# Performance work log

Hardware: AMD Instinct MI355X
Metric: run time of the kernel (lower is better)

The kernel has to match this reference:

```python
import jax, jax.numpy as jnp
import numpy as np
import math

B, L, D, H = 2, 4096, 1024, 16
DH = D // H


def _build_table(seq_len):
    # Faithful port of build_hierarchical_index_lookup_table (static, host-side).
    assert seq_len & (seq_len - 1) == 0
    levels = int(math.log2(seq_len))
    max_valid = 2 * seq_len - 3
    idx = np.full((seq_len, levels), -1, dtype=np.int64)
    cm = np.zeros((seq_len, levels), dtype=bool)
    for n in range(seq_len):
        c = n
        for lvl in range(levels):
            if lvl == 0:
                nxt = c ^ 1
                pair = c
            else:
                nxt = (c // 2 + seq_len) ^ 1
                pair = c // 2 + seq_len
            if nxt > max_valid:
                break
            if pair < nxt:
                cm[n, lvl] = True
            idx[n, lvl] = nxt
            c = nxt
    return idx, cm


def setup_inputs() -> dict:
    rng = jax.random.key(0)
    ks = jax.random.split(rng, 8)
    s = 0.02  # init scale for weights
    idx, cm = _build_table(L)
    return {
        "query": jax.random.normal(ks[0], (B, L, D), jnp.float32),
        "key": jax.random.normal(ks[1], (B, L, D), jnp.float32),
        "value": jax.random.normal(ks[2], (B, L, D), jnp.float32),
        "Wq": jax.random.normal(ks[3], (D, D), jnp.float32) * s,
        "Wk": jax.random.normal(ks[4], (D, D), jnp.float32) * s,
        "Wv": jax.random.normal(ks[5], (D, D), jnp.float32) * s,
        "Wo": jax.random.normal(ks[6], (D, D), jnp.float32) * s,
        "bo": jax.random.normal(ks[7], (D,), jnp.float32) * s,
        "idx_table": jnp.asarray(idx),        # [L, log2(L)] int64
        "causal_mask": jnp.asarray(cm),       # [L, log2(L)] bool
    }


def reference(query, key, value, Wq, Wk, Wv, Wo, bo, idx_table, causal_mask):
    Bq, Lq, Dm = query.shape
    scale = 1.0 / math.sqrt(DH)

    def heads(x, W):  # nn.Linear (no bias) + split heads -> [B,H,L,Dh]
        return (x @ W.T).reshape(Bq, Lq, H, DH).transpose(0, 2, 1, 3)

    Q = heads(query, Wq)
    K = heads(key, Wk)
    V = heads(value, Wv)

    # Build binary-tree hierarchy. Pair weights come from softmax of ZERO
    # logits (Q_parent starts as zeros in the source), so w0 = w1 = 0.5 exactly.
    Ks, Vs = [K], [V]
    while Ks[-1].shape[2] > 1:
        k, v = Ks[-1], Vs[-1]
        Lc = k.shape[2]
        k2 = k.reshape(Bq, H, Lc // 2, 2, DH)
        v2 = v.reshape(Bq, H, Lc // 2, 2, DH)
        Ks.append(0.5 * (k2[:, :, :, 0] + k2[:, :, :, 1]))
        Vs.append(v2[:, :, :, 0] + v2[:, :, :, 1])
    flatK = jnp.concatenate(Ks, axis=2)  # [B,H,2L-1,Dh]
    flatV = jnp.concatenate(Vs, axis=2)

    # Gather neighbor nodes across levels: [B,H,L,levels,Dh]
    nk = flatK[:, :, idx_table]
    nv = flatV[:, :, idx_table]

    self_logits = jnp.einsum('bhnd,bhnd->bhn', Q, K) * scale
    nbr_logits = jnp.einsum('bhld,bhlnd->bhln', Q, nk) * scale
    nbr_logits = jnp.where(causal_mask[None, None], -jnp.inf, nbr_logits)

    all_logits = jnp.concatenate([self_logits[..., None], nbr_logits], axis=-1)
    w = jax.nn.softmax(all_logits, axis=-1)           # [B,H,L,1+levels]
    all_v = jnp.concatenate([V[:, :, :, None, :], nv], axis=3)
    out = jnp.einsum('bhln,bhlnd->bhld', w, all_v)    # [B,H,L,Dh]
    out = out.transpose(0, 2, 1, 3).reshape(Bq, Lq, Dm)
    return out @ Wo.T + bo
```

## Files before the change

kernel.cpp:

```cpp
#include <hip/hip_runtime.h>
#include <cstdint>
#include <cstddef>


typedef __bf16 bf16;
typedef __bf16 bf16x8 __attribute__((ext_vector_type(8)));
typedef __bf16 bf16x4 __attribute__((ext_vector_type(4)));
typedef float  f32x4  __attribute__((ext_vector_type(4)));

#define L_SEQ  4096
#define NFLAT  8192

__device__ __forceinline__ int off_l(int l) { return 8192 - (8192 >> l); }

__device__ __forceinline__ void glds16(const bf16* g, bf16* l) {
  __builtin_amdgcn_global_load_lds(
      (const __attribute__((address_space(1))) unsigned int*)g,
      (__attribute__((address_space(3))) unsigned int*)l, 16, 0, 0);
}

#define MEMFENCE asm volatile("" ::: "memory")
__device__ __forceinline__ void barrier_raw() {
  MEMFENCE; __builtin_amdgcn_s_barrier(); MEMFENCE;
}

__device__ __forceinline__ int swz(int b) { return b ^ (((b >> 9) & 1) << 5); }
__device__ __forceinline__ int la(int row, int col) {
  return ((((row >> 4) << 1) + (col >> 5)) << 10) + ((row & 15) << 6) + ((col & 31) << 1);
}

__global__ __launch_bounds__(256) void cvt3_kernel(
    const float* __restrict__ a, const float* __restrict__ b, const float* __restrict__ c,
    bf16* __restrict__ x, bf16* __restrict__ y, bf16* __restrict__ z) {
  const int s = blockIdx.y;
  const float* src = (s == 0) ? a : (s == 1) ? b : c;
  bf16*        dst = (s == 0) ? x : (s == 1) ? y : z;
  const int i = blockIdx.x * 256 + threadIdx.x;
  const float4 v = ((const float4*)src)[i];
  bf16x4 o;
  o[0] = (bf16)v.x; o[1] = (bf16)v.y; o[2] = (bf16)v.z; o[3] = (bf16)v.w;
  *(bf16x4*)(dst + (size_t)i * 4) = o;
}

__global__ __launch_bounds__(256) void cvt4_kernel(
    const float* __restrict__ a, const float* __restrict__ b,
    const float* __restrict__ c, const float* __restrict__ d,
    bf16* __restrict__ x, bf16* __restrict__ y, bf16* __restrict__ z, bf16* __restrict__ w) {
  const int s = blockIdx.y;
  const float* src = (s == 0) ? a : (s == 1) ? b : (s == 2) ? c : d;
  bf16*        dst = (s == 0) ? x : (s == 1) ? y : (s == 2) ? z : w;
  const int i = blockIdx.x * 256 + threadIdx.x;
  const float4 v = ((const float4*)src)[i];
  bf16x4 o;
  o[0] = (bf16)v.x; o[1] = (bf16)v.y; o[2] = (bf16)v.z; o[3] = (bf16)v.w;
  *(bf16x4*)(dst + (size_t)i * 4) = o;
}

#define BUFB 49152

__device__ __forceinline__ void stage_tile(const bf16* __restrict__ A,
                                           const bf16* __restrict__ W,
                                           int tm, int tn, int k0,
                                           char* buf, int tid, int wid) {
  bf16* Ad = (bf16*)buf;
  bf16* Bd = (bf16*)(buf + 32768);
#pragma unroll
  for (int i = 0; i < 4; i++) {
    const int d  = i * 8192 + tid * 16;
    const int lb = swz(d);
    const int row = ((lb >> 10) >> 1) * 16 + ((lb >> 6) & 15);
    const int col = ((lb >> 10) & 1) * 32 + ((lb & 63) >> 1);
    glds16(A + (size_t)(tm * 256 + row) * 1024 + k0 + col, Ad + (i * 8192 + wid * 1024) / 2);
  }
#pragma unroll
  for (int i = 0; i < 2; i++) {
    const int d  = i * 8192 + tid * 16;
    const int lb = swz(d);
    const int row = ((lb >> 10) >> 1) * 16 + ((lb >> 6) & 15);
    const int col = ((lb >> 10) & 1) * 32 + ((lb & 63) >> 1);
    glds16(W + (size_t)(tn * 128 + row) * 1024 + k0 + col, Bd + (i * 8192 + wid * 1024) / 2);
  }
}

__device__ __forceinline__ void gemm8_core(const bf16* __restrict__ A,
                                           const bf16* __restrict__ W,
                                           int tm, int tn, char* lds,
                                           f32x4 (&acc)[4][4]) {
  const int tid  = threadIdx.x;
  const int wid  = tid >> 6, lane = tid & 63;
  const int wm   = wid >> 1, wn = wid & 1;
  const int laneR  = lane & 15;
  const int laneC8 = (lane >> 4) * 8;

  char* b0 = lds;
  char* b1 = lds + BUFB;
  char* b2 = lds + 2 * BUFB;

  stage_tile(A, W, tm, tn, 0,  b0, tid, wid);
  stage_tile(A, W, tm, tn, 64, b1, tid, wid);

  for (int u = 0; u < 16; ++u) {
    if (u < 15) asm volatile("s_waitcnt vmcnt(6)" ::: "memory");
    else        asm volatile("s_waitcnt vmcnt(0)" ::: "memory");
    barrier_raw();
    if (u + 2 < 16) stage_tile(A, W, tm, tn, (u + 2) << 6, b2, tid, wid);

    const char* Ab = b0;
    const char* Bb = b0 + 32768;
    bf16x8 af[4][2], bfr[4][2];
#pragma unroll
    for (int f = 0; f < 4; f++)
#pragma unroll
      for (int ks = 0; ks < 2; ks++)
        af[f][ks] = *(const bf16x8*)(Ab + swz(la(wm * 64 + f * 16 + laneR, ks * 32 + laneC8)));
#pragma unroll
    for (int j = 0; j < 4; j++)
#pragma unroll
      for (int ks = 0; ks < 2; ks++)
        bfr[j][ks] = *(const bf16x8*)(Bb + swz(la(wn * 64 + j * 16 + laneR, ks * 32 + laneC8)));

    __builtin_amdgcn_s_setprio(1);
#pragma unroll
    for (int f = 0; f < 4; f++)
#pragma unroll
      for (int j = 0; j < 4; j++)
#pragma unroll
        for (int ks = 0; ks < 2; ks++)
          acc[f][j] = __builtin_amdgcn_mfma_f32_16x16x32_bf16(
              af[f][ks], bfr[j][ks], acc[f][j], 0, 0, 0);
    __builtin_amdgcn_s_setprio(0);

    char* t = b0; b0 = b1; b1 = b2; b2 = t;
  }
}

__global__ __launch_bounds__(512, 2) void gemm8_qkv_kernel(
    const bf16* __restrict__ qx, const bf16* __restrict__ kx, const bf16* __restrict__ vx,
    const bf16* __restrict__ wq, const bf16* __restrict__ wk, const bf16* __restrict__ wv,
    bf16* __restrict__ Qb, bf16* __restrict__ fK, bf16* __restrict__ fV) {
  __shared__ __align__(16) char lds[3 * BUFB];
  const int z = blockIdx.y;
  const bf16* A = (z == 0) ? qx : (z == 1) ? kx : vx;
  const bf16* W = (z == 0) ? wq : (z == 1) ? wk : wv;
  bf16* D       = (z == 0) ? Qb : (z == 1) ? fK : fV;
  const int lstr = (z == 0) ? L_SEQ : NFLAT;
  const int tm = blockIdx.x >> 3, tn = blockIdx.x & 7;
  f32x4 acc[4][4] = {};
  gemm8_core(A, W, tm, tn, lds, acc);
  const int lane = threadIdx.x & 63, wid = threadIdx.x >> 6;
  const int m0 = tm * 256 + (wid >> 1) * 64 + (lane >> 4) * 4;
  const int n0 = tn * 128 + (wid & 1) * 64 + (lane & 15);
#pragma unroll
  for (int i = 0; i < 4; i++)
#pragma unroll
    for (int j = 0; j < 4; j++)
#pragma unroll
      for (int r = 0; r < 4; r++) {
        const int m = m0 + i * 16 + r;
        const int n = n0 + j * 16;
        const int b = m >> 12, l = m & 4095;
        const int h = n >> 6,  dh = n & 63;
        D[((size_t)(b * 16 + h) * lstr + l) * 64 + dh] = (bf16)acc[i][j][r];
      }
}

__global__ __launch_bounds__(512, 2) void gemm8_out_kernel(
    const bf16* __restrict__ Ob, const bf16* __restrict__ wo,
    const float* __restrict__ bo, float* __restrict__ out) {
  __shared__ __align__(16) char lds[3 * BUFB];
  const int tm = blockIdx.x >> 3, tn = blockIdx.x & 7;
  f32x4 acc[4][4] = {};
  gemm8_core(Ob, wo, tm, tn, lds, acc);
  const int lane = threadIdx.x & 63, wid = threadIdx.x >> 6;
  const int m0 = tm * 256 + (wid >> 1) * 64 + (lane >> 4) * 4;
  const int n0 = tn * 128 + (wid & 1) * 64 + (lane & 15);
#pragma unroll
  for (int i = 0; i < 4; i++)
#pragma unroll
    for (int j = 0; j < 4; j++)
#pragma unroll
      for (int r = 0; r < 4; r++) {
        const int m = m0 + i * 16 + r;
        const int n = n0 + j * 16;
        out[(size_t)m * 1024 + n] = acc[i][j][r] + bo[n];
      }
}

__global__ __launch_bounds__(64) void tree_l16(bf16* __restrict__ fK, bf16* __restrict__ fV) {
  __shared__ __align__(16) bf16 Kl[64 * 64];
  __shared__ __align__(16) bf16 Vl[64 * 64];
  const int g = blockIdx.x, bh = blockIdx.y;
  const int lane = threadIdx.x;
  const size_t fb = (size_t)bh * NFLAT * 64;
  const size_t leafbase = fb + (size_t)g * 64 * 64;
#pragma unroll
  for (int it = 0; it < 8; it++) {
    glds16(fK + leafbase + it * 512 + lane * 8, Kl + it * 512);
    glds16(fV + leafbase + it * 512 + lane * 8, Vl + it * 512);
  }
  asm volatile("s_waitcnt vmcnt(0)" ::: "memory");
  __syncthreads();

  float pk[7], pv[7];
#pragma unroll
  for (int i = 0; i < 64; i++) {
    float ck = (float)Kl[i * 64 + lane];
    float cv = (float)Vl[i * 64 + lane];
#pragma unroll
    for (int l = 1; l <= 6; l++) {
      if (((i + 1) & ((1 << l) - 1)) != 0) { pk[l] = ck; pv[l] = cv; break; }
      ck += pk[l]; cv += pv[l];
      const int j = (g * 64 + i) >> l;
      fK[fb + (size_t)(off_l(l) + j) * 64 + lane] = (bf16)(ck * (1.0f / (1 << l)));
      fV[fb + (size_t)(off_l(l) + j) * 64 + lane] = (bf16)cv;
    }
  }
}

__global__ __launch_bounds__(64) void tree_l712(bf16* __restrict__ fK, bf16* __restrict__ fV) {
  __shared__ float Ks[64 * 64];
  __shared__ float Vs[64 * 64];
  const int bh = blockIdx.x, d = threadIdx.x;
  const size_t fb = (size_t)bh * NFLAT * 64;
#pragma unroll 8
  for (int i = 0; i < 64; i++) {
    Ks[i * 64 + d] = (float)fK[fb + (size_t)(8064 + i) * 64 + d];
    Vs[i * 64 + d] = (float)fV[fb + (size_t)(8064 + i) * 64 + d];
  }
#pragma unroll
  for (int l = 7; l <= 12; l++) {
    const int cnt = 4096 >> l;
    for (int j = 0; j < cnt; j++) {
      const float k = (Ks[(2 * j) * 64 + d] + Ks[(2 * j + 1) * 64 + d]) * 0.5f;
      const float v =  Vs[(2 * j) * 64 + d] + Vs[(2 * j + 1) * 64 + d];
      Ks[j * 64 + d] = k;
      Vs[j * 64 + d] = v;
      fK[fb + (size_t)(off_l(l) + j) * 64 + d] = (bf16)k;
      fV[fb + (size_t)(off_l(l) + j) * 64 + d] = (bf16)v;
    }
  }
}

__global__ __launch_bounds__(64) void attn_kernel(
    const bf16* __restrict__ Qb, const bf16* __restrict__ fK,
    const bf16* __restrict__ fV, bf16* __restrict__ Ob) {
  __shared__ __align__(16) unsigned short Kl[132 * 64];
  __shared__ __align__(16) unsigned short Vl[132 * 64];
  const int t0  = blockIdx.x * 64;
  const int bh  = blockIdx.y;
  const int tid = threadIdx.x;
  const size_t fb = (size_t)bh * NFLAT * 64;

  for (int u = tid; u < 132 * 8; u += 64) {
    const int r = u >> 3, c = u & 7;
    int flat;
    if      (r < 64)  flat = t0 + r;
    else if (r < 96)  flat = 4096 + (t0 >> 1) + (r - 64);
    else if (r < 112) flat = 6144 + (t0 >> 2) + (r - 96);
    else if (r < 120) flat = 7168 + (t0 >> 3) + (r - 112);
    else if (r < 124) flat = 7680 + (t0 >> 4) + (r - 120);
    else if (r < 126) flat = 7936 + (t0 >> 5) + (r - 124);
    else { const int l = r - 120; flat = (8192 - (8192 >> l) + (t0 >> l)) ^ 1; }
    const int cc = c ^ (r & 7);
    const uint4 kk = *(const uint4*)((const char*)(fK + fb + (size_t)flat * 64) + c * 16);
    const uint4 vv = *(const uint4*)((const char*)(fV + fb + (size_t)flat * 64) + c * 16);
    *(uint4*)((char*)Kl + r * 128 + cc * 16) = kk;
    *(uint4*)((char*)Vl + r * 128 + cc * 16) = vv;
  }
  __syncthreads();

  const int n = t0 + tid;
  int rows[13];
  rows[0] = tid;
#pragma unroll
  for (int l = 0; l < 12; l++) {
    int r;
    if (l == 0)      r = tid ^ 1;
    else if (l <= 5) r = (128 - (128 >> l)) + (((n >> l) ^ 1) - (t0 >> l));
    else             r = 126 + (l - 6);
    rows[l + 1] = r;
  }

  float q[64];
  const bf16* Qr = Qb + ((size_t)bh * L_SEQ + n) * 64;
#pragma unroll
  for (int c = 0; c < 8; c++) {
    bf16x8 v = *(const bf16x8*)(Qr + c * 8);
#pragma unroll
    for (int j = 0; j < 8; j++) q[c * 8 + j] = (float)v[j];
  }

  float lg[13];
#pragma unroll
  for (int v = 0; v < 13; v++) {
    const int r = rows[v];
    float a = 0.f;
#pragma unroll
    for (int c = 0; c < 8; c++) {
      const int cc = c ^ (r & 7);
      const bf16x8 kv = *(const bf16x8*)((const char*)Kl + r * 128 + cc * 16);
#pragma unroll
      for (int j = 0; j < 8; j++) a += q[c * 8 + j] * (float)kv[j];
    }
    lg[v] = a * 0.125f;
  }
#pragma unroll
  for (int v = 1; v < 13; v++)
    if (!((n >> (v - 1)) & 1)) lg[v] = -1e30f;

  float mx = lg[0];
#pragma unroll
  for (int v = 1; v < 13; v++) mx = fmaxf(mx, lg[v]);
  float w[13], s = 0.f;
#pragma unroll
  for (int v = 0; v < 13; v++) { w[v] = __expf(lg[v] - mx); s += w[v]; }
  const float inv = 1.0f / s;

  float o[64];
#pragma unroll
  for (int d = 0; d < 64; d++) o[d] = 0.f;
#pragma unroll
  for (int v = 0; v < 13; v++) {
    const int r = rows[v];
    const float wv = w[v];
#pragma unroll
    for (int c = 0; c < 8; c++) {
      const int cc = c ^ (r & 7);
      const bf16x8 vv = *(const bf16x8*)((const char*)Vl + r * 128 + cc * 16);
#pragma unroll
      for (int j = 0; j < 8; j++) o[c * 8 + j] += wv * (float)vv[j];
    }
  }

  bf16* Or = Ob + ((size_t)(bh >> 4) * L_SEQ + n) * 1024 + (size_t)(bh & 15) * 64;
#pragma unroll
  for (int c = 0; c < 8; c++) {
    bf16x8 ov;
#pragma unroll
    for (int j = 0; j < 8; j++) ov[j] = (bf16)(o[c * 8 + j] * inv);
    *(bf16x8*)(Or + c * 8) = ov;
  }
}

extern "C" void kernel_launch(void* const* d_in, const int* in_sizes, int n_in,
                              void* d_out, int out_size, void* d_ws, size_t ws_size,
                              hipStream_t stream) {
  const float* query = (const float*)d_in[0];
  const float* key   = (const float*)d_in[1];
  const float* value = (const float*)d_in[2];
  const float* Wq    = (const float*)d_in[3];
  const float* Wk    = (const float*)d_in[4];
  const float* Wv    = (const float*)d_in[5];
  const float* Wo    = (const float*)d_in[6];
  const float* bo    = (const float*)d_in[7];
  float* out = (float*)d_out;

  char* ws = (char*)d_ws;
  size_t off = 0;
  auto take = [&](size_t bytes) -> void* {
    void* p = ws + off;
    off += (bytes + 255) & ~(size_t)255;
    return p;
  };
  const size_t XB = (size_t)8192 * 1024 * 2;
  const size_t WB = (size_t)1024 * 1024 * 2;
  bf16* qx  = (bf16*)take(XB);
  bf16* kx  = (bf16*)take(XB);
  bf16* vx  = (bf16*)take(XB);
  bf16* wqx = (bf16*)take(WB);
  bf16* wkx = (bf16*)take(WB);
  bf16* wvx = (bf16*)take(WB);
  bf16* wox = (bf16*)take(WB);
  bf16* Qb  = (bf16*)take((size_t)32 * L_SEQ * 64 * 2);
  bf16* fK  = (bf16*)take((size_t)32 * NFLAT * 64 * 2);
  bf16* fV  = (bf16*)take((size_t)32 * NFLAT * 64 * 2);
  bf16* Ob  = qx;
  (void)in_sizes; (void)n_in; (void)out_size; (void)ws_size;

  cvt3_kernel<<<dim3(8192, 3), 256, 0, stream>>>(query, key, value, qx, kx, vx);
  cvt4_kernel<<<dim3(1024, 4), 256, 0, stream>>>(Wq, Wk, Wv, Wo, wqx, wkx, wvx, wox);

  gemm8_qkv_kernel<<<dim3(256, 3), 512, 0, stream>>>(qx, kx, vx, wqx, wkx, wvx, Qb, fK, fV);

  tree_l16 <<<dim3(64, 32), 64, 0, stream>>>(fK, fV);
  tree_l712<<<32, 64, 0, stream>>>(fK, fV);

  attn_kernel<<<dim3(64, 32), 64, 0, stream>>>(Qb, fK, fV, Ob);

  gemm8_out_kernel<<<256, 512, 0, stream>>>(Ob, wox, bo, out);
}
```

Measured before the change: 185.8 us.

## Shrink GEMM tiles to 128x128 with double buffering and XCD-aware tile mapping

Both projection GEMMs move from 256x128 tiles with 512 threads and triple-buffered LDS to 128x128 tiles with 256 threads and double-buffered LDS, which doubles the grid. Each iteration now waits for all outstanding loads before the barrier instead of keeping one stage in flight. A new tile mapping groups M-tiles by XCD (bid&7) to improve L2 reuse of A rows across N-tiles. The goal is better occupancy and less tail imbalance, at the cost of less load/compute overlap and lower per-tile data reuse.

Measured after the change: 165.3 us. -11.0%, faster.

```diff
diff --git a/kernel.cpp b/kernel.cpp
--- a/kernel.cpp
+++ b/kernel.cpp
@@ -56,29 +56,22 @@
   *(bf16x4*)(dst + (size_t)i * 4) = o;
 }
 
-#define BUFB 49152
+#define BUFB 32768
 
 __device__ __forceinline__ void stage_tile(const bf16* __restrict__ A,
                                            const bf16* __restrict__ W,
                                            int tm, int tn, int k0,
                                            char* buf, int tid, int wid) {
   bf16* Ad = (bf16*)buf;
-  bf16* Bd = (bf16*)(buf + 32768);
+  bf16* Bd = (bf16*)(buf + 16384);
 #pragma unroll
   for (int i = 0; i < 4; i++) {
-    const int d  = i * 8192 + tid * 16;
+    const int d  = i * 4096 + tid * 16;
     const int lb = swz(d);
     const int row = ((lb >> 10) >> 1) * 16 + ((lb >> 6) & 15);
     const int col = ((lb >> 10) & 1) * 32 + ((lb & 63) >> 1);
-    glds16(A + (size_t)(tm * 256 + row) * 1024 + k0 + col, Ad + (i * 8192 + wid * 1024) / 2);
-  }
-#pragma unroll
-  for (int i = 0; i < 2; i++) {
-    const int d  = i * 8192 + tid * 16;
-    const int lb = swz(d);
-    const int row = ((lb >> 10) >> 1) * 16 + ((lb >> 6) & 15);
-    const int col = ((lb >> 10) & 1) * 32 + ((lb & 63) >> 1);
-    glds16(W + (size_t)(tn * 128 + row) * 1024 + k0 + col, Bd + (i * 8192 + wid * 1024) / 2);
+    glds16(A + (size_t)(tm * 128 + row) * 1024 + k0 + col, Ad + ((i * 4096 + wid * 1024) >> 1));
+    glds16(W + (size_t)(tn * 128 + row) * 1024 + k0 + col, Bd + ((i * 4096 + wid * 1024) >> 1));
   }
 }
 
@@ -92,21 +85,16 @@
   const int laneR  = lane & 15;
   const int laneC8 = (lane >> 4) * 8;
 
-  char* b0 = lds;
-  char* b1 = lds + BUFB;
-  char* b2 = lds + 2 * BUFB;
-
-  stage_tile(A, W, tm, tn, 0,  b0, tid, wid);
-  stage_tile(A, W, tm, tn, 64, b1, tid, wid);
+  stage_tile(A, W, tm, tn, 0, lds, tid, wid);
 
   for (int u = 0; u < 16; ++u) {
-    if (u < 15) asm volatile("s_waitcnt vmcnt(6)" ::: "memory");
-    else        asm volatile("s_waitcnt vmcnt(0)" ::: "memory");
+    asm volatile("s_waitcnt vmcnt(0)" ::: "memory");
     barrier_raw();
-    if (u + 2 < 16) stage_tile(A, W, tm, tn, (u + 2) << 6, b2, tid, wid);
-
-    const char* Ab = b0;
-    const char* Bb = b0 + 32768;
+    if (u + 1 < 16)
+      stage_tile(A, W, tm, tn, (u + 1) << 6, lds + ((u + 1) & 1) * BUFB, tid, wid);
+
+    const char* Ab = lds + (u & 1) * BUFB;
+    const char* Bb = Ab + 16384;
     bf16x8 af[4][2], bfr[4][2];
 #pragma unroll
     for (int f = 0; f < 4; f++)
@@ -129,26 +117,30 @@
           acc[f][j] = __builtin_amdgcn_mfma_f32_16x16x32_bf16(
               af[f][ks], bfr[j][ks], acc[f][j], 0, 0, 0);
     __builtin_amdgcn_s_setprio(0);
-
-    char* t = b0; b0 = b1; b1 = b2; b2 = t;
-  }
-}
-
-__global__ __launch_bounds__(512, 2) void gemm8_qkv_kernel(
+  }
+}
+
+__device__ __forceinline__ void tile_map(int bid, int& tm, int& tn) {
+  const int xcd = bid & 7, q = bid >> 3;
+  tm = xcd * 8 + (q >> 3);
+  tn = q & 7;
+}
+
+__global__ __launch_bounds__(256, 2) void gemm8_qkv_kernel(
     const bf16* __restrict__ qx, const bf16* __restrict__ kx, const bf16* __restrict__ vx,
     const bf16* __restrict__ wq, const bf16* __restrict__ wk, const bf16* __restrict__ wv,
     bf16* __restrict__ Qb, bf16* __restrict__ fK, bf16* __restrict__ fV) {
-  __shared__ __align__(16) char lds[3 * BUFB];
+  __shared__ __align__(16) char lds[2 * BUFB];
   const int z = blockIdx.y;
   const bf16* A = (z == 0) ? qx : (z == 1) ? kx : vx;
   const bf16* W = (z == 0) ? wq : (z == 1) ? wk : wv;
   bf16* D       = (z == 0) ? Qb : (z == 1) ? fK : fV;
   const int lstr = (z == 0) ? L_SEQ : NFLAT;
-  const int tm = blockIdx.x >> 3, tn = blockIdx.x & 7;
+  int tm, tn; tile_map(blockIdx.x, tm, tn);
   f32x4 acc[4][4] = {};
   gemm8_core(A, W, tm, tn, lds, acc);
   const int lane = threadIdx.x & 63, wid = threadIdx.x >> 6;
-  const int m0 = tm * 256 + (wid >> 1) * 64 + (lane >> 4) * 4;
+  const int m0 = tm * 128 + (wid >> 1) * 64 + (lane >> 4) * 4;
   const int n0 = tn * 128 + (wid & 1) * 64 + (lane & 15);
 #pragma unroll
   for (int i = 0; i < 4; i++)
@@ -164,15 +156,15 @@
       }
 }
 
-__global__ __launch_bounds__(512, 2) void gemm8_out_kernel(
+__global__ __launch_bounds__(256, 2) void gemm8_out_kernel(
     const bf16* __restrict__ Ob, const bf16* __restrict__ wo,
     const float* __restrict__ bo, float* __restrict__ out) {
-  __shared__ __align__(16) char lds[3 * BUFB];
-  const int tm = blockIdx.x >> 3, tn = blockIdx.x & 7;
+  __shared__ __align__(16) char lds[2 * BUFB];
+  int tm, tn; tile_map(blockIdx.x, tm, tn);
   f32x4 acc[4][4] = {};
   gemm8_core(Ob, wo, tm, tn, lds, acc);
   const int lane = threadIdx.x & 63, wid = threadIdx.x >> 6;
-  const int m0 = tm * 256 + (wid >> 1) * 64 + (lane >> 4) * 4;
+  const int m0 = tm * 128 + (wid >> 1) * 64 + (lane >> 4) * 4;
   const int n0 = tn * 128 + (wid & 1) * 64 + (lane & 15);
 #pragma unroll
   for (int i = 0; i < 4; i++)
@@ -380,12 +372,12 @@
   cvt3_kernel<<<dim3(8192, 3), 256, 0, stream>>>(query, key, value, qx, kx, vx);
   cvt4_kernel<<<dim3(1024, 4), 256, 0, stream>>>(Wq, Wk, Wv, Wo, wqx, wkx, wvx, wox);
 
-  gemm8_qkv_kernel<<<dim3(256, 3), 512, 0, stream>>>(qx, kx, vx, wqx, wkx, wvx, Qb, fK, fV);
+  gemm8_qkv_kernel<<<dim3(512, 3), 256, 0, stream>>>(qx, kx, vx, wqx, wkx, wvx, Qb, fK, fV);
 
   tree_l16 <<<dim3(64, 32), 64, 0, stream>>>(fK, fV);
   tree_l712<<<32, 64, 0, stream>>>(fK, fV);
 
   attn_kernel<<<dim3(64, 32), 64, 0, stream>>>(Qb, fK, fV, Ob);
 
-  gemm8_out_kernel<<<256, 512, 0, stream>>>(Ob, wox, bo, out);
-}
+  gemm8_out_kernel<<<512, 256, 0, stream>>>(Ob, wox, bo, out);
+}
```
